# Kernel optimization log

Measured on AMD Instinct MI355X. Metric: run time of the kernel, lower is better.

## Reference

```python
import jax, jax.numpy as jnp
import numpy as np

BATCH = 8192
IN_F = 4096
OUT_F = 4096


def setup_inputs() -> dict:
    key = jax.random.key(0)
    k_x, k_w, k_m = jax.random.split(key, 3)
    x = jax.random.normal(k_x, (BATCH, IN_F), dtype=jnp.float32)
    # kaiming_normal_ for relu: std = sqrt(2 / fan_in) with fan_in = in_features
    std = float(np.sqrt(2.0 / IN_F))
    weight = jax.random.normal(k_w, (OUT_F, IN_F), dtype=jnp.float32) * std
    bias = jnp.zeros((OUT_F,), dtype=jnp.float32)
    mask = jax.random.bernoulli(k_m, 0.5, (OUT_F, IN_F)).astype(jnp.float32)
    return {"x": x, "weight": weight, "bias": bias, "mask": mask}


def reference(x, weight, bias, mask):
    # masked_weight = weight * mask; out = x @ masked_weight.T + bias
    masked_weight = weight * mask                      # [out, in]
    return jnp.einsum("bi,oi->bo", x, masked_weight) + bias  # [batch, out]
```

## Files before the change

### kernel.cpp

```cpp
#include <hip/hip_runtime.h>
#include <hip/hip_bf16.h>
#include <stdint.h>

#define BATCH 8192
#define IN_F  4096
#define OUT_F 4096

#define BM 128
#define BN 128
#define BK 64

typedef __attribute__((ext_vector_type(8)))  short bf16x8;
typedef __attribute__((ext_vector_type(16))) float f32x16;


__device__ __forceinline__ unsigned short f2bf(float f) {
    unsigned int u = __float_as_uint(f);
    unsigned int lsb = (u >> 16) & 1u;
    u += 0x7fffu + lsb;
    return (unsigned short)(u >> 16);
}

__device__ __forceinline__ void gl_lds16(const void* g, void* l) {
    __builtin_amdgcn_global_load_lds(
        (const __attribute__((address_space(1))) void*)g,
        (__attribute__((address_space(3))) void*)l,
        16, 0, 0);
}

#define XBLK ((BATCH * IN_F) / 8 / 256)
#define WBLK ((OUT_F * IN_F) / 8 / 256)

__global__ __launch_bounds__(256) void cvt_kernel(const float4* __restrict__ x,
                                                  const float4* __restrict__ w,
                                                  const float4* __restrict__ m,
                                                  uint4* __restrict__ xo,
                                                  uint4* __restrict__ wo) {
    int b = blockIdx.x;
    union { unsigned short u[8]; uint4 v; } r;
    if (b < XBLK) {
        int i = b * 256 + threadIdx.x;
        float4 a0 = x[2 * i], a1 = x[2 * i + 1];
        r.u[0] = f2bf(a0.x); r.u[1] = f2bf(a0.y); r.u[2] = f2bf(a0.z); r.u[3] = f2bf(a0.w);
        r.u[4] = f2bf(a1.x); r.u[5] = f2bf(a1.y); r.u[6] = f2bf(a1.z); r.u[7] = f2bf(a1.w);
        xo[i] = r.v;
    } else {
        int i = (b - XBLK) * 256 + threadIdx.x;
        float4 wa = w[2 * i], wb = w[2 * i + 1];
        float4 ma = m[2 * i], mb = m[2 * i + 1];
        r.u[0] = f2bf(wa.x * ma.x); r.u[1] = f2bf(wa.y * ma.y);
        r.u[2] = f2bf(wa.z * ma.z); r.u[3] = f2bf(wa.w * ma.w);
        r.u[4] = f2bf(wb.x * mb.x); r.u[5] = f2bf(wb.y * mb.y);
        r.u[6] = f2bf(wb.z * mb.z); r.u[7] = f2bf(wb.w * mb.w);
        wo[i] = r.v;
    }
}

__global__ __launch_bounds__(256, 4) void gemm_kernel(const unsigned short* __restrict__ A,
                                                      const unsigned short* __restrict__ W,
                                                      const float* __restrict__ bias,
                                                      float* __restrict__ C) {
    __shared__ unsigned short lA[BM * BK];
    __shared__ unsigned short lB[BN * BK];

    const int tid  = threadIdx.x;
    const int lane = tid & 63;
    const int wave = tid >> 6;
    const int bm = blockIdx.y;
    const int bn = blockIdx.x;

    const int wm = (wave & 1) * 64;
    const int wn = (wave >> 1) * 64;
    const int r32 = lane & 31;
    const int hi  = lane >> 5;
    const int swz = lane & 7;

    f32x16 acc[2][2] = {};

    const unsigned short* Ab = A + (size_t)(bm * BM) * IN_F;
    const unsigned short* Wb = W + (size_t)(bn * BN) * IN_F;

    int rowS[4], cgS[4], ldsoff[4];
#pragma unroll
    for (int i = 0; i < 4; ++i) {
        int s = i * 256 + tid;
        rowS[i] = s >> 3;
        cgS[i]  = (s & 7) ^ (rowS[i] & 7);
        ldsoff[i] = s * 8;
    }

    for (int kt = 0; kt < IN_F; kt += BK) {
#pragma unroll
        for (int i = 0; i < 4; ++i) {
            gl_lds16(Ab + (size_t)rowS[i] * IN_F + kt + cgS[i] * 8, &lA[ldsoff[i]]);
            gl_lds16(Wb + (size_t)rowS[i] * IN_F + kt + cgS[i] * 8, &lB[ldsoff[i]]);
        }
        __syncthreads();

#pragma unroll
        for (int ks = 0; ks < 4; ++ks) {
            const int c = ((ks * 2 + hi) ^ swz) * 8;
            bf16x8 af[2], bfj[2];
#pragma unroll
            for (int i = 0; i < 2; ++i)
                af[i] = *(const bf16x8*)&lA[(wm + i * 32 + r32) * BK + c];
#pragma unroll
            for (int j = 0; j < 2; ++j)
                bfj[j] = *(const bf16x8*)&lB[(wn + j * 32 + r32) * BK + c];
#pragma unroll
            for (int i = 0; i < 2; ++i)
#pragma unroll
                for (int j = 0; j < 2; ++j)
                    acc[i][j] = __builtin_amdgcn_mfma_f32_32x32x16_bf16(
                        af[i], bfj[j], acc[i][j], 0, 0, 0);
        }
        __syncthreads();
    }

    const int crow0 = bm * BM + wm;
    const int ccol0 = bn * BN + wn;
#pragma unroll
    for (int j = 0; j < 2; ++j) {
        const int col = ccol0 + j * 32 + r32;
        const float bj = bias[col];
#pragma unroll
        for (int i = 0; i < 2; ++i) {
#pragma unroll
            for (int reg = 0; reg < 16; ++reg) {
                int row = crow0 + i * 32 + (reg & 3) + 8 * (reg >> 2) + 4 * hi;
                C[(size_t)row * OUT_F + col] = acc[i][j][reg] + bj;
            }
        }
    }
}

__global__ __launch_bounds__(256) void fallback_kernel(const float* __restrict__ x,
                                                       const float* __restrict__ w,
                                                       const float* __restrict__ bias,
                                                       const float* __restrict__ m,
                                                       float* __restrict__ out) {
    size_t idx = (size_t)blockIdx.x * 256 + threadIdx.x;
    int row = (int)(idx >> 12);
    int col = (int)(idx & (OUT_F - 1));
    const float4* xr = (const float4*)(x + (size_t)row * IN_F);
    const float4* wr = (const float4*)(w + (size_t)col * IN_F);
    const float4* mr = (const float4*)(m + (size_t)col * IN_F);
    float s = 0.f;
    for (int k = 0; k < IN_F / 4; ++k) {
        float4 xv = xr[k], wv = wr[k], mv = mr[k];
        s += xv.x * wv.x * mv.x + xv.y * wv.y * mv.y +
             xv.z * wv.z * mv.z + xv.w * wv.w * mv.w;
    }
    out[idx] = s + bias[col];
}


extern "C" void kernel_launch(void* const* d_in, const int* in_sizes, int n_in,
                              void* d_out, int out_size, void* d_ws, size_t ws_size,
                              hipStream_t stream) {
    const float* x    = (const float*)d_in[0];
    const float* w    = (const float*)d_in[1];
    const float* bias = (const float*)d_in[2];
    const float* mask = (const float*)d_in[3];
    float* out = (float*)d_out;

    const size_t need = ((size_t)BATCH * IN_F + (size_t)OUT_F * IN_F) * sizeof(unsigned short);
    if (ws_size < need) {
        fallback_kernel<<<(size_t)BATCH * OUT_F / 256, 256, 0, stream>>>(
            x, w, bias, mask, out);
        return;
    }

    unsigned short* xb = (unsigned short*)d_ws;
    unsigned short* wb = xb + (size_t)BATCH * IN_F;

    cvt_kernel<<<XBLK + WBLK, 256, 0, stream>>>(
        (const float4*)x, (const float4*)w, (const float4*)mask,
        (uint4*)xb, (uint4*)wb);

    dim3 grid(OUT_F / BN, BATCH / BM);
    gemm_kernel<<<grid, 256, 0, stream>>>(xb, wb, bias, out);
}
```

Baseline: 589.7 us.

## Rewrite GEMM with 256x256 tiles, double-buffered LDS, 16x16 MFMA and grid swizzle

Replaces the 128x128 single-buffered GEMM with a 256x256 tile handled by 512 threads (8 waves). Global-to-LDS loads are double-buffered so the next K tile is fetched while the current one is computed. Inner products switch to 16x16x32 bf16 MFMA, with s_setprio and explicit waitcnt/barrier scheduling. Block indices are remapped for L2 locality, and the conversion kernel now handles one float4 per thread. This raises reuse per LDS byte and hides load latency, at the cost of more registers and LDS (128 KB), lower occupancy, and fragile hand-tuned sync.

```diff
diff --git a/kernel.cpp b/kernel.cpp
--- a/kernel.cpp
+++ b/kernel.cpp
@@ -1,17 +1,17 @@
 #include <hip/hip_runtime.h>
-#include <hip/hip_bf16.h>
 #include <stdint.h>
 
 #define BATCH 8192
 #define IN_F  4096
 #define OUT_F 4096
 
-#define BM 128
-#define BN 128
+#define BM 256
+#define BN 256
 #define BK 64
-
-typedef __attribute__((ext_vector_type(8)))  short bf16x8;
-typedef __attribute__((ext_vector_type(16))) float f32x16;
+#define KT (IN_F / BK)
+
+typedef __attribute__((ext_vector_type(8))) short bf16x8;
+typedef __attribute__((ext_vector_type(4))) float f32x4;
 
 
 __device__ __forceinline__ unsigned short f2bf(float f) {
@@ -28,109 +28,153 @@
         16, 0, 0);
 }
 
-#define XBLK ((BATCH * IN_F) / 8 / 256)
-#define WBLK ((OUT_F * IN_F) / 8 / 256)
+#define XF4 (BATCH * IN_F / 4)
+#define WF4 (OUT_F * IN_F / 4)
 
 __global__ __launch_bounds__(256) void cvt_kernel(const float4* __restrict__ x,
                                                   const float4* __restrict__ w,
                                                   const float4* __restrict__ m,
-                                                  uint4* __restrict__ xo,
-                                                  uint4* __restrict__ wo) {
-    int b = blockIdx.x;
-    union { unsigned short u[8]; uint4 v; } r;
-    if (b < XBLK) {
-        int i = b * 256 + threadIdx.x;
-        float4 a0 = x[2 * i], a1 = x[2 * i + 1];
-        r.u[0] = f2bf(a0.x); r.u[1] = f2bf(a0.y); r.u[2] = f2bf(a0.z); r.u[3] = f2bf(a0.w);
-        r.u[4] = f2bf(a1.x); r.u[5] = f2bf(a1.y); r.u[6] = f2bf(a1.z); r.u[7] = f2bf(a1.w);
+                                                  uint2* __restrict__ xo,
+                                                  uint2* __restrict__ wo) {
+    const int i = blockIdx.x * 256 + threadIdx.x;
+    union { unsigned short u[4]; uint2 v; } r;
+    if (i < XF4) {
+        const float4 a = x[i];
+        r.u[0] = f2bf(a.x); r.u[1] = f2bf(a.y);
+        r.u[2] = f2bf(a.z); r.u[3] = f2bf(a.w);
         xo[i] = r.v;
     } else {
-        int i = (b - XBLK) * 256 + threadIdx.x;
-        float4 wa = w[2 * i], wb = w[2 * i + 1];
-        float4 ma = m[2 * i], mb = m[2 * i + 1];
-        r.u[0] = f2bf(wa.x * ma.x); r.u[1] = f2bf(wa.y * ma.y);
-        r.u[2] = f2bf(wa.z * ma.z); r.u[3] = f2bf(wa.w * ma.w);
-        r.u[4] = f2bf(wb.x * mb.x); r.u[5] = f2bf(wb.y * mb.y);
-        r.u[6] = f2bf(wb.z * mb.z); r.u[7] = f2bf(wb.w * mb.w);
-        wo[i] = r.v;
-    }
-}
-
-__global__ __launch_bounds__(256, 4) void gemm_kernel(const unsigned short* __restrict__ A,
+        const int j = i - XF4;
+        const float4 a = w[j];
+        const float4 b = m[j];
+        r.u[0] = f2bf(a.x * b.x); r.u[1] = f2bf(a.y * b.y);
+        r.u[2] = f2bf(a.z * b.z); r.u[3] = f2bf(a.w * b.w);
+        wo[j] = r.v;
+    }
+}
+
+__global__ __launch_bounds__(512, 2) void gemm_kernel(const unsigned short* __restrict__ A,
                                                       const unsigned short* __restrict__ W,
                                                       const float* __restrict__ bias,
                                                       float* __restrict__ C) {
-    __shared__ unsigned short lA[BM * BK];
-    __shared__ unsigned short lB[BN * BK];
+    __shared__ unsigned short lA[2][2][128 * BK];
+    __shared__ unsigned short lB[2][2][128 * BK];
 
     const int tid  = threadIdx.x;
     const int lane = tid & 63;
     const int wave = tid >> 6;
-    const int bm = blockIdx.y;
-    const int bn = blockIdx.x;
-
-    const int wm = (wave & 1) * 64;
-    const int wn = (wave >> 1) * 64;
-    const int r32 = lane & 31;
-    const int hi  = lane >> 5;
-    const int swz = lane & 7;
-
-    f32x16 acc[2][2] = {};
-
-    const unsigned short* Ab = A + (size_t)(bm * BM) * IN_F;
-    const unsigned short* Wb = W + (size_t)(bn * BN) * IN_F;
-
-    int rowS[4], cgS[4], ldsoff[4];
+    const int wm   = wave >> 2;
+    const int wn   = wave & 3;
+
+    const int wg = ((blockIdx.x & 7) << 6) | (blockIdx.x >> 3);
+    const int bm = wg >> 4;
+    const int bn = wg & 15;
+
+    const int r15 = lane & 15;
+    const int g   = lane >> 4;
+    const int kx    = ((r15 >> 2) & 1) << 5;
+    const int koff0 = (g * 16) ^ kx;
+
+    int hf[4], ldso[4];
+    const unsigned short* gA[4];
+    const unsigned short* gB[4];
 #pragma unroll
     for (int i = 0; i < 4; ++i) {
-        int s = i * 256 + tid;
-        rowS[i] = s >> 3;
-        cgS[i]  = (s & 7) ^ (rowS[i] & 7);
-        ldsoff[i] = s * 8;
-    }
-
-    for (int kt = 0; kt < IN_F; kt += BK) {
-#pragma unroll
-        for (int i = 0; i < 4; ++i) {
-            gl_lds16(Ab + (size_t)rowS[i] * IN_F + kt + cgS[i] * 8, &lA[ldsoff[i]]);
-            gl_lds16(Wb + (size_t)rowS[i] * IN_F + kt + cgS[i] * 8, &lB[ldsoff[i]]);
+        const int s    = i * 512 + tid;
+        const int h    = s >> 10;
+        const int sl   = s & 1023;
+        const int row  = sl >> 3;
+        const int chnk = (sl & 7) ^ (((sl >> 5) & 1) << 1);
+        hf[i]   = h;
+        ldso[i] = sl * 8;
+        gA[i] = A + (size_t)(bm * BM + h * 128 + row) * IN_F + chnk * 8;
+        gB[i] = W + (size_t)(bn * BN + h * 128 + row) * IN_F + chnk * 8;
+    }
+
+#define STAGE(buf, ktn)                                                 \
+    do {                                                                \
+        _Pragma("unroll")                                               \
+        for (int i = 0; i < 4; ++i) {                                   \
+            gl_lds16(gA[i] + (ktn) * BK, &lA[buf][hf[i]][ldso[i]]);     \
+            gl_lds16(gB[i] + (ktn) * BK, &lB[buf][hf[i]][ldso[i]]);     \
+        }                                                               \
+    } while (0)
+
+    f32x4 acc[8][4] = {};
+
+    STAGE(0, 0);
+    STAGE(1, 1);
+
+    int cur = 0;
+    const int brl = (wn & 1) * 64;
+
+    for (int kt = 0; kt < KT; ++kt) {
+        if (kt + 1 < KT) { asm volatile("s_waitcnt vmcnt(8)" ::: "memory"); }
+        else             { asm volatile("s_waitcnt vmcnt(0)" ::: "memory"); }
+        __builtin_amdgcn_sched_barrier(0);
+        __builtin_amdgcn_s_barrier();
+
+        const char* aB = (const char*)&lA[cur][wm][0];
+        const char* bB = (const char*)&lB[cur][wn >> 1][0];
+
+#pragma unroll
+        for (int p = 0; p < 4; ++p) {
+            const int qm = p >> 1;
+            const int qn = p & 1;
+
+            bf16x8 af[4][2], bg[2][2];
+#pragma unroll
+            for (int ks = 0; ks < 2; ++ks) {
+#pragma unroll
+                for (int fr = 0; fr < 4; ++fr)
+                    af[fr][ks] = *(const bf16x8*)(aB +
+                        (qm * 64 + fr * 16 + r15) * 128 + (koff0 + ks * 64));
+#pragma unroll
+                for (int fc = 0; fc < 2; ++fc)
+                    bg[fc][ks] = *(const bf16x8*)(bB +
+                        (brl + qn * 32 + fc * 16 + r15) * 128 + (koff0 + ks * 64));
+            }
+            __builtin_amdgcn_sched_barrier(0);
+            __builtin_amdgcn_s_barrier();
+            asm volatile("s_waitcnt lgkmcnt(0)" ::: "memory");
+            __builtin_amdgcn_sched_barrier(0);
+
+            __builtin_amdgcn_s_setprio(1);
+#pragma unroll
+            for (int ks = 0; ks < 2; ++ks)
+#pragma unroll
+                for (int fr = 0; fr < 4; ++fr)
+#pragma unroll
+                    for (int fc = 0; fc < 2; ++fc)
+                        acc[qm * 4 + fr][qn * 2 + fc] =
+                            __builtin_amdgcn_mfma_f32_16x16x32_bf16(
+                                af[fr][ks], bg[fc][ks],
+                                acc[qm * 4 + fr][qn * 2 + fc], 0, 0, 0);
+            __builtin_amdgcn_s_setprio(0);
+            __builtin_amdgcn_sched_barrier(0);
+            __builtin_amdgcn_s_barrier();
         }
-        __syncthreads();
-
-#pragma unroll
-        for (int ks = 0; ks < 4; ++ks) {
-            const int c = ((ks * 2 + hi) ^ swz) * 8;
-            bf16x8 af[2], bfj[2];
-#pragma unroll
-            for (int i = 0; i < 2; ++i)
-                af[i] = *(const bf16x8*)&lA[(wm + i * 32 + r32) * BK + c];
-#pragma unroll
-            for (int j = 0; j < 2; ++j)
-                bfj[j] = *(const bf16x8*)&lB[(wn + j * 32 + r32) * BK + c];
-#pragma unroll
-            for (int i = 0; i < 2; ++i)
-#pragma unroll
-                for (int j = 0; j < 2; ++j)
-                    acc[i][j] = __builtin_amdgcn_mfma_f32_32x32x16_bf16(
-                        af[i], bfj[j], acc[i][j], 0, 0, 0);
-        }
-        __syncthreads();
-    }
-
-    const int crow0 = bm * BM + wm;
-    const int ccol0 = bn * BN + wn;
-#pragma unroll
-    for (int j = 0; j < 2; ++j) {
-        const int col = ccol0 + j * 32 + r32;
+
+        __builtin_amdgcn_sched_barrier(0);
+        if (kt + 2 < KT) STAGE(cur, kt + 2);
+        __builtin_amdgcn_sched_barrier(0);
+        cur ^= 1;
+    }
+#undef STAGE
+
+    const int crow0 = bm * BM + wm * 128 + g * 4;
+    const int ccol0 = bn * BN + wn * 64 + r15;
+#pragma unroll
+    for (int nf = 0; nf < 4; ++nf) {
+        const int col = ccol0 + nf * 16;
         const float bj = bias[col];
 #pragma unroll
-        for (int i = 0; i < 2; ++i) {
-#pragma unroll
-            for (int reg = 0; reg < 16; ++reg) {
-                int row = crow0 + i * 32 + (reg & 3) + 8 * (reg >> 2) + 4 * hi;
-                C[(size_t)row * OUT_F + col] = acc[i][j][reg] + bj;
+        for (int mf = 0; mf < 8; ++mf)
+#pragma unroll
+            for (int reg = 0; reg < 4; ++reg) {
+                const int row = crow0 + mf * 16 + reg;
+                C[(size_t)row * OUT_F + col] = acc[mf][nf][reg] + bj;
             }
-        }
     }
 }
 
@@ -174,10 +218,9 @@
     unsigned short* xb = (unsigned short*)d_ws;
     unsigned short* wb = xb + (size_t)BATCH * IN_F;
 
-    cvt_kernel<<<XBLK + WBLK, 256, 0, stream>>>(
+    cvt_kernel<<<(XF4 + WF4) / 256, 256, 0, stream>>>(
         (const float4*)x, (const float4*)w, (const float4*)mask,
-        (uint4*)xb, (uint4*)wb);
-
-    dim3 grid(OUT_F / BN, BATCH / BM);
-    gemm_kernel<<<grid, 256, 0, stream>>>(xb, wb, bias, out);
-}
+        (uint2*)xb, (uint2*)wb);
+
+    gemm_kernel<<<512, 512, 0, stream>>>(xb, wb, bias, out);
+}
```

Result: slower. 749.5 us (+27.1%).
